# Kernel optimization log

Measured on AMD Instinct MI355X. Metric: run time of the kernel, lower is better.

## Reference

```python
import jax, jax.numpy as jnp
import numpy as np

# Directional rectangle cumulative max: max over the axis-aligned rectangle
# between each pixel and one image corner.

def _rectmax(x, rev_h, rev_w):
    y = jax.lax.cummax(x, axis=2, reverse=rev_h)
    return jax.lax.cummax(y, axis=3, reverse=rev_w)


def _guided_pool(xq, gq, rev_h, rev_w):
    # Guided landmark pool: each pixel takes max of itself and the directional
    # cumulative max restricted to guide==1 positions. With guide == ones this
    # reduces to the plain directional rectangle cummax (the un-guided pool).
    neg = jnp.finfo(xq.dtype).min
    masked = jnp.where(gq > 0, xq, neg)
    return jnp.maximum(xq, _rectmax(masked, rev_h, rev_w))

# (rev_h, rev_w) for TopLeft, TopRight, BottomLeft, BottomRight pools
_DIRS = [(True, True), (True, False), (False, True), (False, False)]


def setup_inputs() -> dict:
    key = jax.random.key(0)
    k1, k2, k3 = jax.random.split(key, 3)
    B, C, H, W = 16, 256, 64, 64
    Cout, K = 256, 3
    x = jax.random.normal(k1, (B, C, H, W), jnp.float32)
    weight = jax.random.normal(k2, (Cout, C, K, K), jnp.float32) * 0.02
    bias = jax.random.normal(k3, (Cout,), jnp.float32) * 0.02
    return {"x": x, "weight": weight, "bias": bias}


def reference(x, weight, bias):
    B, C, H, W = x.shape
    Q = C // 4
    # Original torch code squares x IN PLACE via chunk() views before pooling.
    xsq = x * x
    # Per-quadrant channel energy and its global (row, col) argmax -> one-hot guide.
    energy = xsq.reshape(B, 4, Q, H, W).sum(axis=2)            # [B,4,H,W]
    idx = jnp.argmax(energy.reshape(B, 4, H * W), axis=-1)     # [B,4]
    onehot = (jnp.arange(H * W) == idx[..., None]).astype(x.dtype)
    guide = jnp.broadcast_to(onehot.reshape(B, 4, 1, H, W), (B, 4, Q, H, W)).reshape(B, C, H, W)
    # Four directional guided pools, one per channel quadrant, then conv.
    xs = jnp.split(xsq, 4, axis=1)
    gs = jnp.split(guide, 4, axis=1)
    pooled = jnp.concatenate(
        [_guided_pool(xs[i], gs[i], *_DIRS[i]) for i in range(4)], axis=1)
    out = jax.lax.conv_general_dilated(
        pooled, weight, window_strides=(1, 1), padding='SAME',
        dimension_numbers=('NCHW', 'OIHW', 'NCHW'))
    return out + bias[None, :, None, None]
```

## Files before the change

kernel.cpp:

```cpp
#include <hip/hip_runtime.h>
#include <cstddef>

#define B_   16
#define C_   256
#define HW_  4096

typedef __attribute__((ext_vector_type(8)))  short bf16x8;
typedef __attribute__((ext_vector_type(16))) float f32x16;

static __device__ __forceinline__ unsigned short f2bf(float f) {
    unsigned int u = __float_as_uint(f);
    u += 0x7fffu + ((u >> 16) & 1u);
    return (unsigned short)(u >> 16);
}

__global__ __launch_bounds__(256) void fused_energy(const float* __restrict__ x,
                                                    unsigned short* __restrict__ xsqN,
                                                    float* __restrict__ pval,
                                                    int* __restrict__ pidx) {
    int blk = blockIdx.x;
    int b = blk >> 6, h = blk & 63;
    int tid = threadIdx.x;
    int tl  = tid >> 4;
    int w4  = (tid & 15) << 2;
    int wv  = tid >> 6;
    __shared__ float earr[4][4][64];
    __shared__ unsigned short tile[64][264];
    const float* xb = x + (size_t)b * C_ * HW_ + h * 64 + w4;

    float e[4][4];
#pragma unroll
    for (int q = 0; q < 4; ++q)
#pragma unroll
        for (int ww = 0; ww < 4; ++ww) e[q][ww] = 0.f;

#pragma unroll
    for (int i = 0; i < 4; ++i) {
        int c4 = tl * 4 + 64 * i;
        float sq[4][4];
#pragma unroll
        for (int k = 0; k < 4; ++k) {
            float4 v = *(const float4*)(xb + (size_t)(c4 + k) * HW_);
            sq[k][0] = v.x * v.x; sq[k][1] = v.y * v.y;
            sq[k][2] = v.z * v.z; sq[k][3] = v.w * v.w;
            e[i][0] += sq[k][0]; e[i][1] += sq[k][1];
            e[i][2] += sq[k][2]; e[i][3] += sq[k][3];
        }
#pragma unroll
        for (int ww = 0; ww < 4; ++ww) {
            uint2 p;
            p.x = (unsigned)f2bf(sq[0][ww]) | ((unsigned)f2bf(sq[1][ww]) << 16);
            p.y = (unsigned)f2bf(sq[2][ww]) | ((unsigned)f2bf(sq[3][ww]) << 16);
            *(uint2*)(&tile[w4 + ww][c4]) = p;
        }
    }

#pragma unroll
    for (int q = 0; q < 4; ++q)
#pragma unroll
        for (int ww = 0; ww < 4; ++ww) {
            float v = e[q][ww];
            v += __shfl_xor(v, 16);
            v += __shfl_xor(v, 32);
            e[q][ww] = v;
        }
    if ((tid & 48) == 0) {
#pragma unroll
        for (int q = 0; q < 4; ++q) {
            float4 v; v.x = e[q][0]; v.y = e[q][1]; v.z = e[q][2]; v.w = e[q][3];
            *(float4*)&earr[wv][q][w4] = v;
        }
    }
    __syncthreads();

    size_t base = (size_t)(b * 64 + h) * 64 * 256;
#pragma unroll
    for (int it = 0; it < 8; ++it) {
        int row  = it * 8 + (tid >> 5);
        int col8 = (tid & 31) * 8;
        *(int4*)(xsqN + base + (size_t)row * 256 + col8) = *(int4*)&tile[row][col8];
    }

    int q = tid >> 6;
    int w = tid & 63;
    float ev = earr[0][q][w] + earr[1][q][w] + earr[2][q][w] + earr[3][q][w];
    int ix = h * 64 + w;
#pragma unroll
    for (int off = 32; off; off >>= 1) {
        float ov = __shfl_down(ev, off);
        int   oi = __shfl_down(ix, off);
        if (ov > ev || (ov == ev && oi < ix)) { ev = ov; ix = oi; }
    }
    if ((tid & 63) == 0) {
        pval[(b * 64 + h) * 4 + q] = ev;
        pidx[(b * 64 + h) * 4 + q] = ix;
    }
}

__global__ __launch_bounds__(64) void energy_final(const float* __restrict__ pval,
                                                   const int* __restrict__ pidx,
                                                   int* __restrict__ lm,
                                                   const unsigned short* __restrict__ xsqN,
                                                   unsigned short* __restrict__ Lval) {
    int bq = blockIdx.x;
    int b = bq >> 2, q = bq & 3;
    int t = threadIdx.x;
    float ev = pval[(b * 64 + t) * 4 + q];
    int   ix = pidx[(b * 64 + t) * 4 + q];
#pragma unroll
    for (int off = 32; off; off >>= 1) {
        float ov = __shfl_down(ev, off);
        int   oi = __shfl_down(ix, off);
        if (ov > ev || (ov == ev && oi < ix)) { ev = ov; ix = oi; }
    }
    int ix0 = __shfl(ix, 0);
    if (t == 0) lm[bq] = ix0;
    Lval[b * 256 + q * 64 + t] =
        xsqN[((size_t)((b * 64 + (ix0 >> 6)) * 64 + (ix0 & 63))) * 256 + q * 64 + t];
}

__global__ __launch_bounds__(256) void wt_pack(const float* __restrict__ w,
                                               unsigned short* __restrict__ wa) {
    int blk = blockIdx.x;
    int cog = blk >> 3, cib = blk & 7;
    int tid = threadIdx.x;
    __shared__ unsigned short wlds[32][292];
    {
        int co_l = tid >> 3;
        int seg  = tid & 7;
        const float* src = w + ((size_t)((cog * 32 + co_l) * 256 + cib * 32)) * 9 + seg * 36;
#pragma unroll
        for (int f4 = 0; f4 < 9; ++f4) {
            float4 v = *(const float4*)(src + f4 * 4);
            uint2 p;
            p.x = (unsigned)f2bf(v.x) | ((unsigned)f2bf(v.y) << 16);
            p.y = (unsigned)f2bf(v.z) | ((unsigned)f2bf(v.w) << 16);
            *(uint2*)(&wlds[co_l][seg * 36 + f4 * 4]) = p;
        }
    }
    __syncthreads();
    for (int idx = tid; idx < 1152; idx += 256) {
        int lane = idx & 63;
        int s    = (idx >> 6) & 1;
        int j    = idx >> 7;
        int co_l = lane & 31;
        int k0   = s * 16 + (lane >> 5) * 8;
        union { unsigned short us[8]; int4 v; } u;
#pragma unroll
        for (int jj = 0; jj < 8; ++jj)
            u.us[jj] = wlds[co_l][(k0 + jj) * 9 + j];
        int ob = j * 128 + cib * 16 + s * 8 + cog;
        *(int4*)(wa + ((size_t)ob * 64 + lane) * 8) = u.v;
    }
}

__global__ __launch_bounds__(512, 2) void conv_mfma(const unsigned short* __restrict__ xsqN,
                                                    const unsigned short* __restrict__ wa,
                                                    const float* __restrict__ bias,
                                                    const int* __restrict__ lm,
                                                    const unsigned short* __restrict__ Lval,
                                                    float* __restrict__ out) {
    int pt = blockIdx.x;
    int b  = pt >> 4;
    int h0 = (pt & 15) * 4;
    int tid  = threadIdx.x;
    int lane = tid & 63;
    int wv   = tid >> 6;
    int wy = wv >> 2, wx = wv & 3;
    int l31 = lane & 31, qh = lane >> 5;

    __shared__ unsigned short Bs[2][6 * 66 * 40];
    __shared__ unsigned short As[2][8192];

    f32x16 acc[4][2];
#pragma unroll
    for (int mt = 0; mt < 4; ++mt)
#pragma unroll
        for (int nt = 0; nt < 2; ++nt)
#pragma unroll
            for (int r = 0; r < 16; ++r) acc[mt][nt][r] = 0.f;

    int4 sv[4];
    int4 av0, av1;

    {
#pragma unroll
        for (int t2 = 0; t2 < 4; ++t2) {
            int idx = tid + t2 * 512;
            int4 v = {0, 0, 0, 0};
            if (idx < 1584) {
                int pr = idx / 264; int rem = idx - pr * 264;
                int pc = rem >> 2;  int part = rem & 3;
                int grow = h0 - 1 + pr, gcol = pc - 1;
                if ((unsigned)grow < 64u && (unsigned)gcol < 64u)
                    v = *(const int4*)(xsqN + (((size_t)(b * 64 + grow) * 64 + gcol) * 256 + part * 8));
            }
            sv[t2] = v;
        }
        int l = lm[b * 4 + 0];
        int hm = l >> 6, wm = l & 63;
#pragma unroll
        for (int t2 = 0; t2 < 4; ++t2) {
            int idx = tid + t2 * 512;
            if (idx < 1584) {
                int pr = idx / 264; int rem = idx - pr * 264;
                int pc = rem >> 2;  int part = rem & 3;
                int grow = h0 - 1 + pr, gcol = pc - 1;
                union { int4 v; unsigned short us[8]; } u; u.v = sv[t2];
                bool inb = ((unsigned)grow < 64u) && ((unsigned)gcol < 64u);
                if (inb && grow <= hm && gcol <= wm) {
                    union { int4 v; unsigned short us[8]; } Lu;
                    Lu.v = *(const int4*)(Lval + b * 256 + part * 8);
#pragma unroll
                    for (int k = 0; k < 8; ++k)
                        if (Lu.us[k] > u.us[k]) u.us[k] = Lu.us[k];
                }
                *(int4*)(&Bs[0][(pr * 66 + pc) * 40 + part * 8]) = u.v;
            }
        }
        const unsigned short* src = wa + tid * 16;
        av0 = *(const int4*)src;
        av1 = *(const int4*)(src + 8);
        *(int4*)(&As[0][tid * 16])     = av0;
        *(int4*)(&As[0][tid * 16 + 8]) = av1;
    }
    __syncthreads();

    for (int cib = 0; cib < 8; ++cib) {
        for (int j = 0; j < 9; ++j) {
            int p = cib * 9 + j;
            bool hasNext = (p < 71);
            if (hasNext) {
                int jn = j + 1, cibn = cib;
                if (jn == 9) { jn = 0; cibn = cib + 1; }
                const unsigned short* src = wa + ((size_t)(jn * 8 + cibn) << 13) + tid * 16;
                av0 = *(const int4*)src;
                av1 = *(const int4*)(src + 8);
            }
            if (j == 0 && cib < 7) {
                int nc = cib + 1;
#pragma unroll
                for (int t2 = 0; t2 < 4; ++t2) {
                    int idx = tid + t2 * 512;
                    int4 v = {0, 0, 0, 0};
                    if (idx < 1584) {
                        int pr = idx / 264; int rem = idx - pr * 264;
                        int pc = rem >> 2;  int part = rem & 3;
                        int grow = h0 - 1 + pr, gcol = pc - 1;
                        if ((unsigned)grow < 64u && (unsigned)gcol < 64u)
                            v = *(const int4*)(xsqN + (((size_t)(b * 64 + grow) * 64 + gcol) * 256 + nc * 32 + part * 8));
                    }
                    sv[t2] = v;
                }
            }

            {
                const unsigned short* Ab = &As[p & 1][0];
                const unsigned short* Bb = &Bs[cib & 1][0];
                int dh = j / 3 - 1, dw = j % 3 - 1;
                int r  = wx + dh + 1;
                int w0 = l31 + dw + 1;
#pragma unroll
                for (int s = 0; s < 2; ++s) {
                    const bf16x8* ap = (const bf16x8*)(Ab + (((s * 8 + wy * 4) * 64 + lane) << 3));
                    bf16x8 a0 = ap[0];
                    bf16x8 a1 = ap[64];
                    bf16x8 a2 = ap[128];
                    bf16x8 a3 = ap[192];
                    bf16x8 b0 = *(const bf16x8*)(Bb + (r * 66 + w0) * 40 + s * 16 + qh * 8);
                    bf16x8 b1 = *(const bf16x8*)(Bb + (r * 66 + w0 + 32) * 40 + s * 16 + qh * 8);
                    acc[0][0] = __builtin_amdgcn_mfma_f32_32x32x16_bf16(a0, b0, acc[0][0], 0, 0, 0);
                    acc[0][1] = __builtin_amdgcn_mfma_f32_32x32x16_bf16(a0, b1, acc[0][1], 0, 0, 0);
                    acc[1][0] = __builtin_amdgcn_mfma_f32_32x32x16_bf16(a1, b0, acc[1][0], 0, 0, 0);
                    acc[1][1] = __builtin_amdgcn_mfma_f32_32x32x16_bf16(a1, b1, acc[1][1], 0, 0, 0);
                    acc[2][0] = __builtin_amdgcn_mfma_f32_32x32x16_bf16(a2, b0, acc[2][0], 0, 0, 0);
                    acc[2][1] = __builtin_amdgcn_mfma_f32_32x32x16_bf16(a2, b1, acc[2][1], 0, 0, 0);
                    acc[3][0] = __builtin_amdgcn_mfma_f32_32x32x16_bf16(a3, b0, acc[3][0], 0, 0, 0);
                    acc[3][1] = __builtin_amdgcn_mfma_f32_32x32x16_bf16(a3, b1, acc[3][1], 0, 0, 0);
                }
            }

            if (j == 8 && cib < 7) {
                int nc = cib + 1;
                int l = lm[b * 4 + (nc >> 1)];
                int hm = l >> 6, wm = l & 63;
                bool qhle = (nc >> 1) < 2;
                bool qwle = ((nc >> 1) & 1) == 0;
                unsigned short* Bw = &Bs[(cib + 1) & 1][0];
#pragma unroll
                for (int t2 = 0; t2 < 4; ++t2) {
                    int idx = tid + t2 * 512;
                    if (idx < 1584) {
                        int pr = idx / 264; int rem = idx - pr * 264;
                        int pc = rem >> 2;  int part = rem & 3;
                        int grow = h0 - 1 + pr, gcol = pc - 1;
                        union { int4 v; unsigned short us[8]; } u; u.v = sv[t2];
                        bool inb = ((unsigned)grow < 64u) && ((unsigned)gcol < 64u);
                        bool hok = qhle ? (grow <= hm) : (grow >= hm);
                        bool wok = qwle ? (gcol <= wm) : (gcol >= wm);
                        if (inb && hok && wok) {
                            union { int4 v; unsigned short us[8]; } Lu;
                            Lu.v = *(const int4*)(Lval + b * 256 + nc * 32 + part * 8);
#pragma unroll
                            for (int k = 0; k < 8; ++k)
                                if (Lu.us[k] > u.us[k]) u.us[k] = Lu.us[k];
                        }
                        *(int4*)(&Bw[(pr * 66 + pc) * 40 + part * 8]) = u.v;
                    }
                }
            }
            if (hasNext) {
                unsigned short* dst = &As[(p + 1) & 1][tid * 16];
                *(int4*)dst       = av0;
                *(int4*)(dst + 8) = av1;
            }
            __syncthreads();
        }
    }

    int h = h0 + wx;
#pragma unroll
    for (int mt = 0; mt < 4; ++mt) {
#pragma unroll
        for (int nt = 0; nt < 2; ++nt) {
#pragma unroll
            for (int r = 0; r < 16; ++r) {
                int row = (r & 3) + 8 * (r >> 2) + 4 * qh;
                int co  = wy * 128 + mt * 32 + row;
                int w   = nt * 32 + l31;
                out[(((size_t)(b * 256 + co)) * 64 + h) * 64 + w] = acc[mt][nt][r] + bias[co];
            }
        }
    }
}

extern "C" void kernel_launch(void* const* d_in, const int* in_sizes, int n_in,
                              void* d_out, int out_size, void* d_ws, size_t ws_size,
                              hipStream_t stream) {
    const float* x      = (const float*)d_in[0];
    const float* weight = (const float*)d_in[1];
    const float* bias   = (const float*)d_in[2];
    float* out = (float*)d_out;

    char* ws = (char*)d_ws;
    int*            lmp  = (int*)ws;
    float*          pval = (float*)(ws + 256);
    int*            pidx = (int*)(ws + 256 + 16384);
    unsigned short* Lval = (unsigned short*)(ws + 256 + 32768);
    unsigned short* Wa   = (unsigned short*)(ws + 49152);
    unsigned short* xsqN = (unsigned short*)(ws + 49152 + 1179648);

    hipLaunchKernelGGL(fused_energy, dim3(1024), dim3(256), 0, stream, x, xsqN, pval, pidx);
    hipLaunchKernelGGL(energy_final, dim3(64), dim3(64), 0, stream, pval, pidx, lmp, xsqN, Lval);
    hipLaunchKernelGGL(wt_pack, dim3(64), dim3(256), 0, stream, weight, Wa);
    hipLaunchKernelGGL(conv_mfma, dim3(256), dim3(512), 0, stream, xsqN, Wa, bias, lmp, Lval, out);
}
```

Before: 196.2 us.

## Stage three conv taps per barrier with direct global-to-LDS weight loads

The weight-packing kernel now lays weights out as (cib, tap) contiguous, so one phase covers three taps. The conv main loop processes three 3x3 taps per __syncthreads instead of one, cutting the barriers from 72 to 24. Weights are copied with global_load_lds straight into a larger triple-sized A buffer, skipping the register round trip. LDS use per block rises substantially (A buffer tripled), which may reduce occupancy at the requested two blocks per CU.

```diff
diff --git a/kernel.cpp b/kernel.cpp
--- a/kernel.cpp
+++ b/kernel.cpp
@@ -149,8 +149,58 @@
 #pragma unroll
         for (int jj = 0; jj < 8; ++jj)
             u.us[jj] = wlds[co_l][(k0 + jj) * 9 + j];
-        int ob = j * 128 + cib * 16 + s * 8 + cog;
+        int ob = (cib * 9 + j) * 16 + s * 8 + cog;
         *(int4*)(wa + ((size_t)ob * 64 + lane) * 8) = u.v;
+    }
+}
+
+static __device__ __forceinline__ void load_B(int4 sv[4],
+                                              const unsigned short* __restrict__ xsqN,
+                                              int b, int h0, int nc, int tid) {
+#pragma unroll
+    for (int t2 = 0; t2 < 4; ++t2) {
+        int idx = tid + t2 * 512;
+        int4 v = {0, 0, 0, 0};
+        if (idx < 1584) {
+            int pr = idx / 264; int rem = idx - pr * 264;
+            int pc = rem >> 2;  int part = rem & 3;
+            int grow = h0 - 1 + pr, gcol = pc - 1;
+            if ((unsigned)grow < 64u && (unsigned)gcol < 64u)
+                v = *(const int4*)(xsqN + (((size_t)(b * 64 + grow) * 64 + gcol) * 256 + nc * 32 + part * 8));
+        }
+        sv[t2] = v;
+    }
+}
+
+static __device__ __forceinline__ void store_B(const int4 sv[4],
+                                               unsigned short* __restrict__ Bw,
+                                               const unsigned short* __restrict__ Lval,
+                                               const int* __restrict__ lm,
+                                               int b, int h0, int nc, int tid) {
+    int l = lm[b * 4 + (nc >> 1)];
+    int hm = l >> 6, wm = l & 63;
+    bool qhle = (nc >> 1) < 2;
+    bool qwle = ((nc >> 1) & 1) == 0;
+#pragma unroll
+    for (int t2 = 0; t2 < 4; ++t2) {
+        int idx = tid + t2 * 512;
+        if (idx < 1584) {
+            int pr = idx / 264; int rem = idx - pr * 264;
+            int pc = rem >> 2;  int part = rem & 3;
+            int grow = h0 - 1 + pr, gcol = pc - 1;
+            union { int4 v; unsigned short us[8]; } u; u.v = sv[t2];
+            bool inb = ((unsigned)grow < 64u) && ((unsigned)gcol < 64u);
+            bool hok = qhle ? (grow <= hm) : (grow >= hm);
+            bool wok = qwle ? (gcol <= wm) : (gcol >= wm);
+            if (inb && hok && wok) {
+                union { int4 v; unsigned short us[8]; } Lu;
+                Lu.v = *(const int4*)(Lval + b * 256 + nc * 32 + part * 8);
+#pragma unroll
+                for (int k = 0; k < 8; ++k)
+                    if (Lu.us[k] > u.us[k]) u.us[k] = Lu.us[k];
+            }
+            *(int4*)(&Bw[(pr * 66 + pc) * 40 + part * 8]) = u.v;
+        }
     }
 }
 
@@ -170,7 +220,7 @@
     int l31 = lane & 31, qh = lane >> 5;
 
     __shared__ unsigned short Bs[2][6 * 66 * 40];
-    __shared__ unsigned short As[2][8192];
+    __shared__ unsigned short As[2][3 * 8192];
 
     f32x16 acc[4][2];
 #pragma unroll
@@ -181,94 +231,50 @@
             for (int r = 0; r < 16; ++r) acc[mt][nt][r] = 0.f;
 
     int4 sv[4];
-    int4 av0, av1;
-
+
+    load_B(sv, xsqN, b, h0, 0, tid);
     {
-#pragma unroll
-        for (int t2 = 0; t2 < 4; ++t2) {
-            int idx = tid + t2 * 512;
-            int4 v = {0, 0, 0, 0};
-            if (idx < 1584) {
-                int pr = idx / 264; int rem = idx - pr * 264;
-                int pc = rem >> 2;  int part = rem & 3;
-                int grow = h0 - 1 + pr, gcol = pc - 1;
-                if ((unsigned)grow < 64u && (unsigned)gcol < 64u)
-                    v = *(const int4*)(xsqN + (((size_t)(b * 64 + grow) * 64 + gcol) * 256 + part * 8));
+        const unsigned short* s0 = wa + wv * 3072 + lane * 8;
+#pragma unroll
+        for (int k = 0; k < 6; ++k)
+            __builtin_amdgcn_global_load_lds(s0 + k * 512, &As[0][wv * 3072 + k * 512], 16, 0, 0);
+    }
+    store_B(sv, &Bs[0][0], Lval, lm, b, h0, 0, tid);
+    __syncthreads();
+
+    for (int cib = 0; cib < 8; ++cib) {
+#pragma unroll
+        for (int sub = 0; sub < 3; ++sub) {
+            int ph = cib * 3 + sub;
+
+            if (ph < 23) {
+                const unsigned short* s0 = wa + (size_t)(ph + 1) * 24576 + wv * 3072 + lane * 8;
+                unsigned short* d0 = &As[(ph + 1) & 1][wv * 3072];
+#pragma unroll
+                for (int k = 0; k < 6; ++k)
+                    __builtin_amdgcn_global_load_lds(s0 + k * 512, d0 + k * 512, 16, 0, 0);
             }
-            sv[t2] = v;
-        }
-        int l = lm[b * 4 + 0];
-        int hm = l >> 6, wm = l & 63;
-#pragma unroll
-        for (int t2 = 0; t2 < 4; ++t2) {
-            int idx = tid + t2 * 512;
-            if (idx < 1584) {
-                int pr = idx / 264; int rem = idx - pr * 264;
-                int pc = rem >> 2;  int part = rem & 3;
-                int grow = h0 - 1 + pr, gcol = pc - 1;
-                union { int4 v; unsigned short us[8]; } u; u.v = sv[t2];
-                bool inb = ((unsigned)grow < 64u) && ((unsigned)gcol < 64u);
-                if (inb && grow <= hm && gcol <= wm) {
-                    union { int4 v; unsigned short us[8]; } Lu;
-                    Lu.v = *(const int4*)(Lval + b * 256 + part * 8);
-#pragma unroll
-                    for (int k = 0; k < 8; ++k)
-                        if (Lu.us[k] > u.us[k]) u.us[k] = Lu.us[k];
-                }
-                *(int4*)(&Bs[0][(pr * 66 + pc) * 40 + part * 8]) = u.v;
-            }
-        }
-        const unsigned short* src = wa + tid * 16;
-        av0 = *(const int4*)src;
-        av1 = *(const int4*)(src + 8);
-        *(int4*)(&As[0][tid * 16])     = av0;
-        *(int4*)(&As[0][tid * 16 + 8]) = av1;
-    }
-    __syncthreads();
-
-    for (int cib = 0; cib < 8; ++cib) {
-        for (int j = 0; j < 9; ++j) {
-            int p = cib * 9 + j;
-            bool hasNext = (p < 71);
-            if (hasNext) {
-                int jn = j + 1, cibn = cib;
-                if (jn == 9) { jn = 0; cibn = cib + 1; }
-                const unsigned short* src = wa + ((size_t)(jn * 8 + cibn) << 13) + tid * 16;
-                av0 = *(const int4*)src;
-                av1 = *(const int4*)(src + 8);
-            }
-            if (j == 0 && cib < 7) {
-                int nc = cib + 1;
-#pragma unroll
-                for (int t2 = 0; t2 < 4; ++t2) {
-                    int idx = tid + t2 * 512;
-                    int4 v = {0, 0, 0, 0};
-                    if (idx < 1584) {
-                        int pr = idx / 264; int rem = idx - pr * 264;
-                        int pc = rem >> 2;  int part = rem & 3;
-                        int grow = h0 - 1 + pr, gcol = pc - 1;
-                        if ((unsigned)grow < 64u && (unsigned)gcol < 64u)
-                            v = *(const int4*)(xsqN + (((size_t)(b * 64 + grow) * 64 + gcol) * 256 + nc * 32 + part * 8));
-                    }
-                    sv[t2] = v;
-                }
-            }
-
-            {
-                const unsigned short* Ab = &As[p & 1][0];
-                const unsigned short* Bb = &Bs[cib & 1][0];
-                int dh = j / 3 - 1, dw = j % 3 - 1;
-                int r  = wx + dh + 1;
-                int w0 = l31 + dw + 1;
+            if (sub == 0 && cib < 7)
+                load_B(sv, xsqN, b, h0, cib + 1, tid);
+
+            const unsigned short* Ab = &As[ph & 1][0];
+            const unsigned short* Bb = &Bs[cib & 1][0];
+#pragma unroll
+            for (int tt = 0; tt < 3; ++tt) {
+                int j  = sub * 3 + tt;
+                int r  = wx + j / 3;
+                int w0 = l31 + j % 3;
+                const unsigned short* Bp = Bb + (r * 66 + w0) * 40 + qh * 8;
+                const unsigned short* At = Ab + tt * 8192;
 #pragma unroll
                 for (int s = 0; s < 2; ++s) {
-                    const bf16x8* ap = (const bf16x8*)(Ab + (((s * 8 + wy * 4) * 64 + lane) << 3));
+                    const bf16x8* ap = (const bf16x8*)(At + (((s * 8 + wy * 4) * 64 + lane) << 3));
                     bf16x8 a0 = ap[0];
                     bf16x8 a1 = ap[64];
                     bf16x8 a2 = ap[128];
                     bf16x8 a3 = ap[192];
-                    bf16x8 b0 = *(const bf16x8*)(Bb + (r * 66 + w0) * 40 + s * 16 + qh * 8);
-                    bf16x8 b1 = *(const bf16x8*)(Bb + (r * 66 + w0 + 32) * 40 + s * 16 + qh * 8);
+                    bf16x8 b0 = *(const bf16x8*)(Bp + s * 16);
+                    bf16x8 b1 = *(const bf16x8*)(Bp + 1280 + s * 16);
                     acc[0][0] = __builtin_amdgcn_mfma_f32_32x32x16_bf16(a0, b0, acc[0][0], 0, 0, 0);
                     acc[0][1] = __builtin_amdgcn_mfma_f32_32x32x16_bf16(a0, b1, acc[0][1], 0, 0, 0);
                     acc[1][0] = __builtin_amdgcn_mfma_f32_32x32x16_bf16(a1, b0, acc[1][0], 0, 0, 0);
@@ -280,40 +286,9 @@
                 }
             }
 
-            if (j == 8 && cib < 7) {
-                int nc = cib + 1;
-                int l = lm[b * 4 + (nc >> 1)];
-                int hm = l >> 6, wm = l & 63;
-                bool qhle = (nc >> 1) < 2;
-                bool qwle = ((nc >> 1) & 1) == 0;
-                unsigned short* Bw = &Bs[(cib + 1) & 1][0];
-#pragma unroll
-                for (int t2 = 0; t2 < 4; ++t2) {
-                    int idx = tid + t2 * 512;
-                    if (idx < 1584) {
-                        int pr = idx / 264; int rem = idx - pr * 264;
-                        int pc = rem >> 2;  int part = rem & 3;
-                        int grow = h0 - 1 + pr, gcol = pc - 1;
-                        union { int4 v; unsigned short us[8]; } u; u.v = sv[t2];
-                        bool inb = ((unsigned)grow < 64u) && ((unsigned)gcol < 64u);
-                        bool hok = qhle ? (grow <= hm) : (grow >= hm);
-                        bool wok = qwle ? (gcol <= wm) : (gcol >= wm);
-                        if (inb && hok && wok) {
-                            union { int4 v; unsigned short us[8]; } Lu;
-                            Lu.v = *(const int4*)(Lval + b * 256 + nc * 32 + part * 8);
-#pragma unroll
-                            for (int k = 0; k < 8; ++k)
-                                if (Lu.us[k] > u.us[k]) u.us[k] = Lu.us[k];
-                        }
-                        *(int4*)(&Bw[(pr * 66 + pc) * 40 + part * 8]) = u.v;
-                    }
-                }
-            }
-            if (hasNext) {
-                unsigned short* dst = &As[(p + 1) & 1][tid * 16];
-                *(int4*)dst       = av0;
-                *(int4*)(dst + 8) = av1;
-            }
+            if (sub == 2 && cib < 7)
+                store_B(sv, &Bs[(cib + 1) & 1][0], Lval, lm, b, h0, cib + 1, tid);
+
             __syncthreads();
         }
     }
```

Result: faster. 189.5 us (-3.4%).
